# Optimization experiments

Hardware: AMD Instinct MI355X
Metric: run time of the kernel (lower is better)

Reference implementation:

```python
import jax, jax.numpy as jnp
import numpy as np

N_NODES = 50000
N_EDGES = 800000
HIDDEN = 128
HEADS = 8
HEAD_DIM = HIDDEN // HEADS
N_REL = 64
SCALE = np.sqrt(HEAD_DIM).astype(np.float32)


def setup_inputs() -> dict:
    key = jax.random.key(0)
    ks = jax.random.split(key, 12)
    s = 1.0 / np.sqrt(2 * HIDDEN)
    s2 = 1.0 / np.sqrt(HIDDEN)
    return {
        "node_features": jax.random.normal(ks[0], (N_NODES, HIDDEN), jnp.float32),
        "query_embedding": jax.random.normal(ks[1], (1, HIDDEN), jnp.float32),
        "relation_embeddings": jax.random.normal(ks[2], (N_REL, HIDDEN), jnp.float32),
        "Wq": jax.random.uniform(ks[3], (2 * HIDDEN, HIDDEN), jnp.float32, -s, s),
        "bq": jnp.zeros((HIDDEN,), jnp.float32),
        "Wk": jax.random.uniform(ks[4], (2 * HIDDEN, HIDDEN), jnp.float32, -s, s),
        "bk": jnp.zeros((HIDDEN,), jnp.float32),
        "Wv": jax.random.uniform(ks[5], (HIDDEN, HIDDEN), jnp.float32, -s2, s2),
        "bv": jnp.zeros((HIDDEN,), jnp.float32),
        "Wo": jax.random.uniform(ks[6], (HIDDEN, HIDDEN), jnp.float32, -s2, s2),
        "bo": jnp.zeros((HIDDEN,), jnp.float32),
        "edge_index": jax.random.randint(ks[7], (2, N_EDGES), 0, N_NODES, jnp.int64),
        "edge_type": jax.random.randint(ks[8], (N_EDGES,), 0, N_REL, jnp.int64),
    }


def reference(node_features, query_embedding, relation_embeddings,
              Wq, bq, Wk, bk, Wv, bv, Wo, bo, edge_index, edge_type):
    n = node_features.shape[0]
    # expand query to all nodes and concat: [N, 2*hidden]
    q_exp = jnp.broadcast_to(query_embedding, (n, HIDDEN))
    nq = jnp.concatenate([node_features, q_exp], axis=-1)
    q = (nq @ Wq + bq).reshape(n, HEADS, HEAD_DIM)
    k = (nq @ Wk + bk).reshape(n, HEADS, HEAD_DIM)
    v = (node_features @ Wv + bv).reshape(n, HEADS, HEAD_DIM)

    src, dst = edge_index[0], edge_index[1]
    rel_bias = relation_embeddings[edge_type].reshape(-1, HEADS, HEAD_DIM)

    # edge-wise scores [E, heads]
    scores = jnp.sum(q[dst] * (k[src] + rel_bias), axis=-1) / SCALE

    # sparse softmax grouped by dst; torch init of max buffer is 0 -> clamp at 0
    seg_max = jax.ops.segment_max(scores, dst, num_segments=n)
    seg_max = jnp.maximum(seg_max, 0.0)
    exp_s = jnp.exp(scores - seg_max[dst])
    seg_sum = jax.ops.segment_sum(exp_s, dst, num_segments=n)
    attn = exp_s / (seg_sum[dst] + 1e-8)  # [E, heads]

    messages = attn[:, :, None] * v[src]  # [E, heads, head_dim]
    out = jax.ops.segment_sum(messages, dst, num_segments=n)  # [N, heads, head_dim]
    out = out.reshape(n, HIDDEN)
    return out @ Wo + bo
```

## Files before the change

kernel.cpp:

```cpp
#include <hip/hip_runtime.h>
#include <math.h>

#define N_NODES 50000
#define N_EDGES 800000
#define HID 128
#define HEADS 8
#define HDIM 16
#define CNT_BLOCKS 3125
#define QKV_BLOCKS 782

typedef __attribute__((ext_vector_type(8))) short short8;
typedef __attribute__((ext_vector_type(4))) float floatx4;

#if defined(__has_builtin)
#if __has_builtin(__builtin_amdgcn_fdot2_f32_bf16)
#define HAVE_DOT2 1
#endif
#endif
#ifndef HAVE_DOT2
#define HAVE_DOT2 0
#endif

#if HAVE_DOT2
typedef __attribute__((ext_vector_type(2))) __bf16 bf16x2;
__device__ __forceinline__ float dot2acc(unsigned int a, unsigned int b, float c) {
    return __builtin_amdgcn_fdot2_f32_bf16(__builtin_bit_cast(bf16x2, a),
                                           __builtin_bit_cast(bf16x2, b), c, false);
}
#endif

__device__ __forceinline__ float bf_lo(unsigned int d) { return __uint_as_float(d << 16); }
__device__ __forceinline__ float bf_hi(unsigned int d) { return __uint_as_float(d & 0xFFFF0000u); }
__device__ __forceinline__ unsigned short f2bf(float f) {
    unsigned int u = __float_as_uint(f);
    u = (u + 0x7FFFu + ((u >> 16) & 1u)) >> 16;
    return (unsigned short)u;
}
__device__ __forceinline__ unsigned int pack_bf2(float a, float b) {
    return (unsigned int)f2bf(a) | ((unsigned int)f2bf(b) << 16);
}

__global__ __launch_bounds__(256) void prep_count_kernel(
    const float* __restrict__ query, const float* __restrict__ rel,
    const float* __restrict__ Wq, const float* __restrict__ bq,
    const float* __restrict__ Wk, const float* __restrict__ bk,
    const float* __restrict__ Wv, const float* __restrict__ Wo,
    const int* __restrict__ ei,
    unsigned short* __restrict__ Wt, unsigned short* __restrict__ relbf,
    int* __restrict__ counts, int* __restrict__ epos,
    float* __restrict__ bqe, float* __restrict__ bke) {
    int b = blockIdx.x;
    if (b < CNT_BLOCKS) {
        int e = b * 256 + threadIdx.x;
        if (e < N_EDGES) epos[e] = atomicAdd(&counts[ei[N_EDGES + e]], 1);
        return;
    }
    b -= CNT_BLOCKS;
    if (b == 256) {
        int j = threadIdx.x;
        if (j < HID) {
            float aq = bq[j], ak = bk[j];
            for (int i = 0; i < HID; ++i) {
                float qv = query[i];
                aq += qv * Wq[(HID + i) * HID + j];
                ak += qv * Wk[(HID + i) * HID + j];
            }
            bqe[j] = aq;
            bke[j] = ak;
        }
        return;
    }
    int idx = b * 256 + threadIdx.x;
    if (idx < 64 * HID) relbf[idx] = f2bf(rel[idx]);
    int m = idx >> 14;
    int rem = idx & 16383;
    int n = rem >> 7, k = rem & 127;
    const float* W = (m == 0) ? Wq : (m == 1) ? Wk : (m == 2) ? Wv : Wo;
    Wt[idx] = f2bf(W[k * HID + n]);
}

__global__ __launch_bounds__(256) void scan1_kernel(const int* __restrict__ counts,
                                                    int* __restrict__ row_start,
                                                    int* __restrict__ bsums) {
    __shared__ int wsum[4];
    int b = blockIdx.x, tid = threadIdx.x, lane = tid & 63, w = tid >> 6;
    int i0 = b * 1024 + tid * 4;
    int x0 = (i0 + 0 < N_NODES) ? counts[i0 + 0] : 0;
    int x1 = (i0 + 1 < N_NODES) ? counts[i0 + 1] : 0;
    int x2 = (i0 + 2 < N_NODES) ? counts[i0 + 2] : 0;
    int x3 = (i0 + 3 < N_NODES) ? counts[i0 + 3] : 0;
    int t = x0 + x1 + x2 + x3;
    int val = t;
    #pragma unroll
    for (int off = 1; off < 64; off <<= 1) {
        int y = __shfl_up(val, off);
        if (lane >= off) val += y;
    }
    if (lane == 63) wsum[w] = val;
    __syncthreads();
    int wo = 0;
    if (w > 0) wo += wsum[0];
    if (w > 1) wo += wsum[1];
    if (w > 2) wo += wsum[2];
    int excl = wo + val - t;
    if (i0 + 0 < N_NODES) row_start[i0 + 0] = excl;
    if (i0 + 1 < N_NODES) row_start[i0 + 1] = excl + x0;
    if (i0 + 2 < N_NODES) row_start[i0 + 2] = excl + x0 + x1;
    if (i0 + 3 < N_NODES) row_start[i0 + 3] = excl + x0 + x1 + x2;
    if (tid == 255) bsums[b] = wo + val;
}

__global__ __launch_bounds__(256) void scan23_kernel(int* __restrict__ row_start,
                                                     const int* __restrict__ bsums) {
    __shared__ int soff;
    int b = blockIdx.x, tid = threadIdx.x;
    if (tid < 64) {
        int x = (tid < b) ? bsums[tid] : 0;
        #pragma unroll
        for (int off = 32; off > 0; off >>= 1) x += __shfl_down(x, off);
        if (tid == 0) soff = x;
    }
    __syncthreads();
    int off = soff;
    int i0 = b * 1024 + tid * 4;
    if (i0 + 3 < N_NODES) {
        int4* p = (int4*)(row_start + i0);
        int4 v = *p;
        v.x += off; v.y += off; v.z += off; v.w += off;
        *p = v;
    } else {
        for (int j = 0; j < 4; ++j)
            if (i0 + j < N_NODES) row_start[i0 + j] += off;
    }
    if (b == 0 && tid == 0) row_start[N_NODES] = N_EDGES;
}

__global__ __launch_bounds__(256) void qkv_scatter_kernel(
    const float* __restrict__ nf, const unsigned short* __restrict__ Wt,
    const float* __restrict__ bqe, const float* __restrict__ bke, const float* __restrict__ bv,
    const int* __restrict__ ei, const int* __restrict__ et,
    const int* __restrict__ row_start, const int* __restrict__ epos,
    unsigned short* __restrict__ qb16, unsigned short* __restrict__ kv16,
    unsigned int* __restrict__ csr) {
    if (blockIdx.x >= QKV_BLOCKS) {
        int e = (blockIdx.x - QKV_BLOCKS) * 256 + threadIdx.x;
        if (e < N_EDGES) {
            int dst = ei[N_EDGES + e];
            csr[row_start[dst] + epos[e]] = ((unsigned int)et[e] << 18) | (unsigned int)ei[e];
        }
        return;
    }
    int row0 = blockIdx.x * 64;
    int wave = threadIdx.x >> 6;
    int lane = threadIdx.x & 63;
    int col  = lane & 15;
    int quad = lane >> 4;

    short8 afr[4][4];
    #pragma unroll
    for (int t = 0; t < 4; ++t) {
        int arow = row0 + t * 16 + col;
        int asafe = (arow < N_NODES) ? arow : (N_NODES - 1);
        #pragma unroll
        for (int kk = 0; kk < 4; ++kk) {
            const float4* ap = (const float4*)(nf + (size_t)asafe * HID + kk * 32 + quad * 8);
            float4 a0 = ap[0], a1 = ap[1];
            short8 f;
            f[0] = (short)f2bf(a0.x); f[1] = (short)f2bf(a0.y);
            f[2] = (short)f2bf(a0.z); f[3] = (short)f2bf(a0.w);
            f[4] = (short)f2bf(a1.x); f[5] = (short)f2bf(a1.y);
            f[6] = (short)f2bf(a1.z); f[7] = (short)f2bf(a1.w);
            afr[t][kk] = f;
        }
    }

    const float* biases[3] = {bqe, bke, bv};
    #pragma unroll
    for (int m = 0; m < 3; ++m) {
        const unsigned short* W = Wt + (size_t)m * HID * HID;
        #pragma unroll
        for (int nn = 0; nn < 2; ++nn) {
            int n = wave * 2 + nn;
            float b = biases[m][n * 16 + col];
            floatx4 acc[4];
            #pragma unroll
            for (int t = 0; t < 4; ++t) acc[t] = (floatx4){b, b, b, b};
            short8 bfr[4];
            #pragma unroll
            for (int kk = 0; kk < 4; ++kk)
                bfr[kk] = *(const short8*)(W + (size_t)(n * 16 + col) * HID + kk * 32 + quad * 8);
            #pragma unroll
            for (int kk = 0; kk < 4; ++kk)
                #pragma unroll
                for (int t = 0; t < 4; ++t)
                    acc[t] = __builtin_amdgcn_mfma_f32_16x16x32_bf16(afr[t][kk], bfr[kk], acc[t], 0, 0, 0);
            #pragma unroll
            for (int t = 0; t < 4; ++t) {
                #pragma unroll
                for (int i = 0; i < 4; ++i) {
                    int r = row0 + t * 16 + quad * 4 + i;
                    if (r < N_NODES) {
                        int c = n * 16 + col;
                        if (m == 0)      qb16[(size_t)r * HID + c] = f2bf(acc[t][i]);
                        else if (m == 1) kv16[(size_t)r * 256 + c] = f2bf(acc[t][i]);
                        else             kv16[(size_t)r * 256 + 128 + c] = f2bf(acc[t][i]);
                    }
                }
            }
        }
    }
}

__global__ __launch_bounds__(256) void out_mfma_kernel(
    const unsigned short* __restrict__ abuf, const unsigned short* __restrict__ Wot,
    const float* __restrict__ bo, float* __restrict__ out) {
    int row0 = blockIdx.x * 64;
    int wave = threadIdx.x >> 6;
    int lane = threadIdx.x & 63;
    int col  = lane & 15;
    int quad = lane >> 4;

    short8 afr[4][4];
    #pragma unroll
    for (int t = 0; t < 4; ++t) {
        int arow = row0 + t * 16 + col;
        int asafe = (arow < N_NODES) ? arow : (N_NODES - 1);
        #pragma unroll
        for (int kk = 0; kk < 4; ++kk)
            afr[t][kk] = *(const short8*)(abuf + (size_t)asafe * HID + kk * 32 + quad * 8);
    }

    #pragma unroll
    for (int nn = 0; nn < 2; ++nn) {
        int n = wave * 2 + nn;
        float b = bo[n * 16 + col];
        floatx4 acc[4];
        #pragma unroll
        for (int t = 0; t < 4; ++t) acc[t] = (floatx4){b, b, b, b};
        short8 bfr[4];
        #pragma unroll
        for (int kk = 0; kk < 4; ++kk)
            bfr[kk] = *(const short8*)(Wot + (size_t)(n * 16 + col) * HID + kk * 32 + quad * 8);
        #pragma unroll
        for (int kk = 0; kk < 4; ++kk)
            #pragma unroll
            for (int t = 0; t < 4; ++t)
                acc[t] = __builtin_amdgcn_mfma_f32_16x16x32_bf16(afr[t][kk], bfr[kk], acc[t], 0, 0, 0);
        #pragma unroll
        for (int t = 0; t < 4; ++t) {
            #pragma unroll
            for (int i = 0; i < 4; ++i) {
                int r = row0 + t * 16 + quad * 4 + i;
                if (r < N_NODES) out[(size_t)r * HID + n * 16 + col] = acc[t][i];
            }
        }
    }
}

__global__ __launch_bounds__(256) void attn_kernel(
    const unsigned int* __restrict__ qb, const unsigned int* __restrict__ kvu,
    const float* __restrict__ rel, const unsigned int* __restrict__ relu,
    const int* __restrict__ row_start, const unsigned int* __restrict__ csr,
    unsigned int* __restrict__ abuf) {
    int node = blockIdx.x * 4 + (threadIdx.x >> 6);
    int lane = threadIdx.x & 63;
    int h = lane & 7;
    int hd = lane >> 3;
    int rs = row_start[node];
    int deg = row_start[node + 1] - rs;

    const uint4* qp = (const uint4*)(qb + (size_t)node * 64 + h * 8);
    uint4 qa = qp[0], qc = qp[1];
#if !HAVE_DOT2
    float qf0 = bf_lo(qa.x), qf1 = bf_hi(qa.x), qf2 = bf_lo(qa.y), qf3 = bf_hi(qa.y);
    float qf4 = bf_lo(qa.z), qf5 = bf_hi(qa.z), qf6 = bf_lo(qa.w), qf7 = bf_hi(qa.w);
    float qf8 = bf_lo(qc.x), qf9 = bf_hi(qc.x), qf10 = bf_lo(qc.y), qf11 = bf_hi(qc.y);
    float qf12 = bf_lo(qc.z), qf13 = bf_hi(qc.z), qf14 = bf_lo(qc.w), qf15 = bf_hi(qc.w);
#endif

    int myel = lane >> 3;
    unsigned int pk = (myel < deg) ? csr[rs + myel] : 0u;
    float ssum = 0.0f, accx = 0.0f, accy = 0.0f;
    for (int base = 0; base < deg; base += 8) {
        int el = base + myel;
        int eln = el + 8;
        unsigned int pk_next = (eln < deg) ? csr[rs + eln] : 0u;
        float w = 0.0f;
        int src = 0;
        if (el < deg) {
            src = pk & 0x3FFFF;
            int etv = (int)(pk >> 18);
            const uint4* kp = (const uint4*)(kvu + (size_t)src * 128 + h * 8);
            uint4 ka = kp[0], kb = kp[1];
            float s;
#if HAVE_DOT2
            const uint4* rp = (const uint4*)(relu + (size_t)etv * 64 + h * 8);
            uint4 ra = rp[0], rb = rp[1];
            float s0 = dot2acc(qa.x, ka.x, 0.0f);
            float s1 = dot2acc(qa.y, ka.y, 0.0f);
            float s2 = dot2acc(qa.z, ka.z, 0.0f);
            float s3 = dot2acc(qa.w, ka.w, 0.0f);
            s0 = dot2acc(qc.x, kb.x, s0);
            s1 = dot2acc(qc.y, kb.y, s1);
            s2 = dot2acc(qc.z, kb.z, s2);
            s3 = dot2acc(qc.w, kb.w, s3);
            s0 = dot2acc(qa.x, ra.x, s0);
            s1 = dot2acc(qa.y, ra.y, s1);
            s2 = dot2acc(qa.z, ra.z, s2);
            s3 = dot2acc(qa.w, ra.w, s3);
            s0 = dot2acc(qc.x, rb.x, s0);
            s1 = dot2acc(qc.y, rb.y, s1);
            s2 = dot2acc(qc.z, rb.z, s2);
            s3 = dot2acc(qc.w, rb.w, s3);
            s = (s0 + s1) + (s2 + s3);
#else
            const float4* rp = (const float4*)(rel + (size_t)etv * HID + h * HDIM);
            float4 r0 = rp[0], r1 = rp[1], r2 = rp[2], r3 = rp[3];
            float s0 = qf0 * (bf_lo(ka.x) + r0.x) + qf4 * (bf_lo(ka.z) + r1.x)
                     + qf8 * (bf_lo(kb.x) + r2.x) + qf12 * (bf_lo(kb.z) + r3.x);
            float s1 = qf1 * (bf_hi(ka.x) + r0.y) + qf5 * (bf_hi(ka.z) + r1.y)
                     + qf9 * (bf_hi(kb.x) + r2.y) + qf13 * (bf_hi(kb.z) + r3.y);
            float s2 = qf2 * (bf_lo(ka.y) + r0.z) + qf6 * (bf_lo(ka.w) + r1.z)
                     + qf10 * (bf_lo(kb.y) + r2.z) + qf14 * (bf_lo(kb.w) + r3.z);
            float s3 = qf3 * (bf_hi(ka.y) + r0.w) + qf7 * (bf_hi(ka.w) + r1.w)
                     + qf11 * (bf_hi(kb.y) + r2.w) + qf15 * (bf_hi(kb.w) + r3.w);
            s = (s0 + s1) + (s2 + s3);
#endif
            w = __expf(s * 0.25f);
            ssum += w;
        }
        #pragma unroll
        for (int j = 0; j < 8; ++j) {
            int   sj = __shfl(src, j * 8);
            float wj = __shfl(w, j * 8 + hd);
            unsigned int vp = kvu[(size_t)sj * 128 + 64 + lane];
            accx += wj * bf_lo(vp);
            accy += wj * bf_hi(vp);
        }
        pk = pk_next;
    }
    #pragma unroll
    for (int off = 8; off < 64; off <<= 1) ssum += __shfl_xor(ssum, off);
    float inv = 1.0f / (__shfl(ssum, hd) + 1e-8f);
    abuf[(size_t)node * 64 + lane] = pack_bf2(accx * inv, accy * inv);
}

extern "C" void kernel_launch(void* const* d_in, const int* in_sizes, int n_in,
                              void* d_out, int out_size, void* d_ws, size_t ws_size,
                              hipStream_t stream) {
    const float* nf    = (const float*)d_in[0];
    const float* query = (const float*)d_in[1];
    const float* rel   = (const float*)d_in[2];
    const float* Wq    = (const float*)d_in[3];
    const float* bq    = (const float*)d_in[4];
    const float* Wk    = (const float*)d_in[5];
    const float* bk    = (const float*)d_in[6];
    const float* Wv    = (const float*)d_in[7];
    const float* bv    = (const float*)d_in[8];
    const float* Wo    = (const float*)d_in[9];
    const float* bo    = (const float*)d_in[10];
    const int*   ei    = (const int*)d_in[11];
    const int*   et    = (const int*)d_in[12];
    float* out = (float*)d_out;

    char* ws = (char*)d_ws;
    unsigned short* qb16 = (unsigned short*)ws; ws += (size_t)N_NODES * HID * 2;
    unsigned short* kv16 = (unsigned short*)ws; ws += (size_t)N_NODES * 256 * 2;
    unsigned int* abuf   = (unsigned int*)ws;   ws += (size_t)N_NODES * 64 * 4;
    float* bqe           = (float*)ws;          ws += 128 * 4;
    float* bke           = (float*)ws;          ws += 128 * 4;
    int* row_start       = (int*)ws;            ws += (size_t)(N_NODES + 4) * 4;
    int* counts          = (int*)ws;            ws += (size_t)N_NODES * 4;
    int* epos            = (int*)ws;            ws += (size_t)N_EDGES * 4;
    int* bsums           = (int*)ws;            ws += 64 * 4;
    unsigned int* csr    = (unsigned int*)ws;   ws += (size_t)N_EDGES * 4;
    unsigned short* Wt   = (unsigned short*)ws; ws += (size_t)4 * HID * HID * 2;
    unsigned short* relbf = (unsigned short*)ws; ws += (size_t)64 * HID * 2;

    const int SCAN_BLOCKS = (N_NODES + 1023) / 1024;

    hipMemsetAsync(counts, 0, (size_t)N_NODES * 4, stream);
    prep_count_kernel<<<CNT_BLOCKS + 257, 256, 0, stream>>>(
        query, rel, Wq, bq, Wk, bk, Wv, Wo, ei, Wt, relbf, counts, epos, bqe, bke);
    scan1_kernel<<<SCAN_BLOCKS, 256, 0, stream>>>(counts, row_start, bsums);
    scan23_kernel<<<SCAN_BLOCKS, 256, 0, stream>>>(row_start, bsums);
    qkv_scatter_kernel<<<QKV_BLOCKS + CNT_BLOCKS, 256, 0, stream>>>(
        nf, Wt, bqe, bke, bv, ei, et, row_start, epos, qb16, kv16, csr);
    attn_kernel<<<N_NODES / 4, 256, 0, stream>>>(
        (const unsigned int*)qb16, (const unsigned int*)kv16, rel,
        (const unsigned int*)relbf, row_start, csr, abuf);
    out_mfma_kernel<<<QKV_BLOCKS, 256, 0, stream>>>(
        (const unsigned short*)abuf, Wt + (size_t)3 * HID * HID, bo, out);
}
```

Baseline: 247.4 us.

## Split each node's edge loop across two waves with LDS reduction

The attention kernel now gives each destination node two wavefronts. Each wave takes alternating groups of 8 edges, and the partial accumulators and softmax sums are combined through shared memory after a block barrier. This shortens the serial edge loop per wave and roughly halves the latency of the dependent gathers for the typical degree of about 16. The edge weight is rounded to bf16 and packed with a 16-bit source index, so one shuffle replaces two. Index math moves to 32-bit, and the csr software prefetch is dropped. The costs are a __syncthreads, LDS traffic, a slightly less precise attention weight, and an implicit assumption that node ids fit in 16 bits.

New measurement: 246.0 us. About the same (-0.5%).

```diff
diff --git a/kernel.cpp b/kernel.cpp
--- a/kernel.cpp
+++ b/kernel.cpp
@@ -259,17 +259,21 @@
 
 __global__ __launch_bounds__(256) void attn_kernel(
     const unsigned int* __restrict__ qb, const unsigned int* __restrict__ kvu,
-    const float* __restrict__ rel, const unsigned int* __restrict__ relu,
+    const unsigned int* __restrict__ relu,
     const int* __restrict__ row_start, const unsigned int* __restrict__ csr,
     unsigned int* __restrict__ abuf) {
-    int node = blockIdx.x * 4 + (threadIdx.x >> 6);
+    __shared__ float lds_acc[2][64][2];
+    __shared__ float lds_ssum[2][2][8];
+    int slot = threadIdx.x >> 7;
+    int wv   = (threadIdx.x >> 6) & 1;
+    int node = blockIdx.x * 2 + slot;
     int lane = threadIdx.x & 63;
     int h = lane & 7;
     int hd = lane >> 3;
     int rs = row_start[node];
     int deg = row_start[node + 1] - rs;
 
-    const uint4* qp = (const uint4*)(qb + (size_t)node * 64 + h * 8);
+    const uint4* qp = (const uint4*)(qb + (unsigned)node * 64 + h * 8);
     uint4 qa = qp[0], qc = qp[1];
 #if !HAVE_DOT2
     float qf0 = bf_lo(qa.x), qf1 = bf_hi(qa.x), qf2 = bf_lo(qa.y), qf3 = bf_hi(qa.y);
@@ -278,24 +282,21 @@
     float qf12 = bf_lo(qc.z), qf13 = bf_hi(qc.z), qf14 = bf_lo(qc.w), qf15 = bf_hi(qc.w);
 #endif
 
-    int myel = lane >> 3;
-    unsigned int pk = (myel < deg) ? csr[rs + myel] : 0u;
+    int myel0 = wv * 8 + (lane >> 3);
     float ssum = 0.0f, accx = 0.0f, accy = 0.0f;
-    for (int base = 0; base < deg; base += 8) {
-        int el = base + myel;
-        int eln = el + 8;
-        unsigned int pk_next = (eln < deg) ? csr[rs + eln] : 0u;
-        float w = 0.0f;
-        int src = 0;
+    for (int base = 0; base < deg; base += 16) {
+        int el = base + myel0;
+        unsigned int pw = 0u;
         if (el < deg) {
-            src = pk & 0x3FFFF;
-            int etv = (int)(pk >> 18);
-            const uint4* kp = (const uint4*)(kvu + (size_t)src * 128 + h * 8);
+            unsigned int pk = csr[rs + el];
+            unsigned int src = pk & 0x3FFFF;
+            unsigned int etv = pk >> 18;
+            const uint4* kp = (const uint4*)(kvu + (src << 7) + h * 8);
             uint4 ka = kp[0], kb = kp[1];
+            const uint4* rp = (const uint4*)(relu + (etv << 6) + h * 8);
+            uint4 ra = rp[0], rb = rp[1];
             float s;
 #if HAVE_DOT2
-            const uint4* rp = (const uint4*)(relu + (size_t)etv * 64 + h * 8);
-            uint4 ra = rp[0], rb = rp[1];
             float s0 = dot2acc(qa.x, ka.x, 0.0f);
             float s1 = dot2acc(qa.y, ka.y, 0.0f);
             float s2 = dot2acc(qa.z, ka.z, 0.0f);
@@ -314,35 +315,45 @@
             s3 = dot2acc(qc.w, rb.w, s3);
             s = (s0 + s1) + (s2 + s3);
 #else
-            const float4* rp = (const float4*)(rel + (size_t)etv * HID + h * HDIM);
-            float4 r0 = rp[0], r1 = rp[1], r2 = rp[2], r3 = rp[3];
-            float s0 = qf0 * (bf_lo(ka.x) + r0.x) + qf4 * (bf_lo(ka.z) + r1.x)
-                     + qf8 * (bf_lo(kb.x) + r2.x) + qf12 * (bf_lo(kb.z) + r3.x);
-            float s1 = qf1 * (bf_hi(ka.x) + r0.y) + qf5 * (bf_hi(ka.z) + r1.y)
-                     + qf9 * (bf_hi(kb.x) + r2.y) + qf13 * (bf_hi(kb.z) + r3.y);
-            float s2 = qf2 * (bf_lo(ka.y) + r0.z) + qf6 * (bf_lo(ka.w) + r1.z)
-                     + qf10 * (bf_lo(kb.y) + r2.z) + qf14 * (bf_lo(kb.w) + r3.z);
-            float s3 = qf3 * (bf_hi(ka.y) + r0.w) + qf7 * (bf_hi(ka.w) + r1.w)
-                     + qf11 * (bf_hi(kb.y) + r2.w) + qf15 * (bf_hi(kb.w) + r3.w);
+            float s0 = qf0 * (bf_lo(ka.x) + bf_lo(ra.x)) + qf4 * (bf_lo(ka.z) + bf_lo(ra.z))
+                     + qf8 * (bf_lo(kb.x) + bf_lo(rb.x)) + qf12 * (bf_lo(kb.z) + bf_lo(rb.z));
+            float s1 = qf1 * (bf_hi(ka.x) + bf_hi(ra.x)) + qf5 * (bf_hi(ka.z) + bf_hi(ra.z))
+                     + qf9 * (bf_hi(kb.x) + bf_hi(rb.x)) + qf13 * (bf_hi(kb.z) + bf_hi(rb.z));
+            float s2 = qf2 * (bf_lo(ka.y) + bf_lo(ra.y)) + qf6 * (bf_lo(ka.w) + bf_lo(ra.w))
+                     + qf10 * (bf_lo(kb.y) + bf_lo(rb.y)) + qf14 * (bf_lo(kb.w) + bf_lo(rb.w));
+            float s3 = qf3 * (bf_hi(ka.y) + bf_hi(ra.y)) + qf7 * (bf_hi(ka.w) + bf_hi(ra.w))
+                     + qf11 * (bf_hi(kb.y) + bf_hi(rb.y)) + qf15 * (bf_hi(kb.w) + bf_hi(rb.w));
             s = (s0 + s1) + (s2 + s3);
 #endif
-            w = __expf(s * 0.25f);
+            float w = __expf(s * 0.25f);
+            unsigned int wb = (unsigned int)f2bf(w);
+            w = __uint_as_float(wb << 16);
             ssum += w;
+            pw = (wb << 16) | src;
         }
         #pragma unroll
         for (int j = 0; j < 8; ++j) {
-            int   sj = __shfl(src, j * 8);
-            float wj = __shfl(w, j * 8 + hd);
-            unsigned int vp = kvu[(size_t)sj * 128 + 64 + lane];
+            unsigned int pj = __shfl(pw, j * 8 + hd);
+            float wj = bf_hi(pj);
+            unsigned int sj = pj & 0xFFFFu;
+            unsigned int vp = kvu[(sj << 7) + 64 + lane];
             accx += wj * bf_lo(vp);
             accy += wj * bf_hi(vp);
         }
-        pk = pk_next;
     }
     #pragma unroll
     for (int off = 8; off < 64; off <<= 1) ssum += __shfl_xor(ssum, off);
-    float inv = 1.0f / (__shfl(ssum, hd) + 1e-8f);
-    abuf[(size_t)node * 64 + lane] = pack_bf2(accx * inv, accy * inv);
+
+    if (lane < 8) lds_ssum[slot][wv][lane] = ssum;
+    if (wv == 1) { lds_acc[slot][lane][0] = accx; lds_acc[slot][lane][1] = accy; }
+    __syncthreads();
+    if (wv == 0) {
+        accx += lds_acc[slot][lane][0];
+        accy += lds_acc[slot][lane][1];
+        float stot = lds_ssum[slot][0][hd] + lds_ssum[slot][1][hd];
+        float inv = 1.0f / (stot + 1e-8f);
+        abuf[(unsigned)node * 64 + lane] = pack_bf2(accx * inv, accy * inv);
+    }
 }
 
 extern "C" void kernel_launch(void* const* d_in, const int* in_sizes, int n_in,
@@ -386,8 +397,8 @@
     scan23_kernel<<<SCAN_BLOCKS, 256, 0, stream>>>(row_start, bsums);
     qkv_scatter_kernel<<<QKV_BLOCKS + CNT_BLOCKS, 256, 0, stream>>>(
         nf, Wt, bqe, bke, bv, ei, et, row_start, epos, qb16, kv16, csr);
-    attn_kernel<<<N_NODES / 4, 256, 0, stream>>>(
-        (const unsigned int*)qb16, (const unsigned int*)kv16, rel,
+    attn_kernel<<<N_NODES / 2, 256, 0, stream>>>(
+        (const unsigned int*)qb16, (const unsigned int*)kv16,
         (const unsigned int*)relbf, row_start, csr, abuf);
     out_mfma_kernel<<<QKV_BLOCKS, 256, 0, stream>>>(
         (const unsigned short*)abuf, Wt + (size_t)3 * HID * HID, bo, out);
```
